# Kernel tuning notes

Hardware: AMD Instinct MI355X
Metric: run time of the kernel (lower is better)

## Reference

```python
import math
import jax, jax.numpy as jnp
import numpy as np

EPS = 1e-6
MAX_SCALE_LOG = math.log(100.0)

def rms_norm(x, scale, eps=EPS):
    # x * scale / rms(x), reduction over last dim
    ms = jnp.mean(jnp.square(x), axis=-1, keepdims=True)
    return x * (scale * jax.lax.rsqrt(ms + eps))

def axial_rope_theta(pos, n_heads, d_head, dtype):
    # freqs: linspace in log-space from pi to 10*pi, reshaped to [n_heads, d_head//4]
    f = np.exp(np.linspace(math.log(math.pi), math.log(10.0 * math.pi),
                           n_heads * d_head // 4 + 1)[:-1])
    freqs = jnp.asarray(f.reshape(d_head // 4, n_heads).T, dtype)  # [h, e/4]
    theta_h = pos[:, :, None, 0:1] * freqs  # [n, l, h, e/4]
    theta_w = pos[:, :, None, 1:2] * freqs  # [n, l, h, e/4]
    theta = jnp.concatenate([theta_h, theta_w], axis=-1)  # [n, l, h, e/2]
    return theta.transpose(0, 2, 1, 3)  # [n, h, l, e/2]

def apply_rotary(x, theta):
    d = theta.shape[-1]
    x1, x2, x3 = x[..., :d], x[..., d:2 * d], x[..., 2 * d:]
    cos, sin = jnp.cos(theta), jnp.sin(theta)
    return jnp.concatenate([x1 * cos - x2 * sin, x2 * cos + x1 * sin, x3], axis=-1)

def setup_inputs() -> dict:
    key = jax.random.key(0)
    ks = jax.random.split(key, 8)
    n, l, d_model, d_head = 2, 2048, 1024, 64
    n_heads = d_model // d_head
    x = jax.random.normal(ks[0], (n, l, d_model), jnp.float32)
    pos = jax.random.uniform(ks[1], (n, l, 2), jnp.float32)
    cond = jax.random.normal(ks[2], (n, 1, d_model), jnp.float32)
    # params (torch uses zero-init for w_cond/w_out; small random for a non-degenerate baseline)
    w_cond = jax.random.normal(ks[3], (d_model, d_model), jnp.float32) * 0.02
    w_qkv = jax.random.normal(ks[4], (d_model, 3 * d_model), jnp.float32) * (d_model ** -0.5)
    qk_scale = jnp.full((n_heads,), math.log(10.0), jnp.float32)
    w_out = jax.random.normal(ks[5], (d_model, d_model), jnp.float32) * 0.02
    return {"x": x, "pos": pos, "cond": cond, "w_cond": w_cond,
            "w_qkv": w_qkv, "qk_scale": qk_scale, "w_out": w_out}

def reference(x, pos, cond, w_cond, w_qkv, qk_scale, w_out):
    n, l, d_model = x.shape
    h = qk_scale.shape[0]
    e = d_model // h
    # AdaRMSNorm: scale = linear(cond) + 1
    xn = rms_norm(x, cond @ w_cond + 1.0)
    # QKV projection
    q, k, v = jnp.split(xn @ w_qkv, 3, axis=-1)
    to_heads = lambda t: t.reshape(n, l, h, e).transpose(0, 2, 1, 3)  # [n,h,l,e]
    q, k, v = to_heads(q), to_heads(k), to_heads(v)
    # QKNorm: per-head learned scale, rms over head dim
    s = jnp.exp(0.5 * jnp.minimum(qk_scale, MAX_SCALE_LOG) - 0.25 * math.log(e))
    q = rms_norm(q, s[:, None, None])
    k = rms_norm(k, s[:, None, None])
    # Axial RoPE
    theta = axial_rope_theta(pos, h, e, x.dtype)
    q = apply_rotary(q, theta)
    k = apply_rotary(k, theta)
    # SDPA (no mask)
    attn = jax.nn.softmax(jnp.einsum('nhqe,nhke->nhqk', q, k) / math.sqrt(e), axis=-1)
    o = jnp.einsum('nhqk,nhke->nhqe', attn, v)
    o = o.transpose(0, 2, 1, 3).reshape(n, l, d_model)
    return o @ w_out
```

## Files before the change

kernel.cpp:

```cpp
#include <hip/hip_runtime.h>

typedef unsigned short u16;
typedef unsigned int u32;
typedef short s16x8 __attribute__((ext_vector_type(8)));
typedef short s16x4 __attribute__((ext_vector_type(4)));
typedef float f32x4 __attribute__((ext_vector_type(4)));
typedef u32 u32x2 __attribute__((ext_vector_type(2)));

#define AS1 __attribute__((address_space(1)))
#define AS3 __attribute__((address_space(3)))

__device__ __forceinline__ float bf2f(u16 u) {
    union { unsigned int i; float f; } x; x.i = ((unsigned int)u) << 16; return x.f;
}
__device__ __forceinline__ u16 f2bf(float f) {
    union { float f; unsigned int i; } x; x.f = f;
    unsigned int r = (x.i + 0x7FFFu + ((x.i >> 16) & 1u)) >> 16;
    return (u16)r;
}
__device__ __forceinline__ void storeOut(u16* p, float v) { *p = f2bf(v); }
__device__ __forceinline__ void storeOut(float* p, float v) { *p = v; }
__device__ __forceinline__ float loadIn(const void* p, size_t i, int isf32) {
    return isf32 ? ((const float*)p)[i] : bf2f(((const u16*)p)[i]);
}
__device__ __forceinline__ float fexp2(float x) {
#if __has_builtin(__builtin_amdgcn_exp2f)
    return __builtin_amdgcn_exp2f(x);
#else
    return exp2f(x);
#endif
}
__device__ __forceinline__ u32 pack_bf(float a, float b) {
    u32 ua = __float_as_uint(a) + 0x8000u;
    u32 ub = __float_as_uint(b) + 0x8000u;
    return __builtin_amdgcn_perm(ub, ua, 0x07060302u);
}

__global__ __launch_bounds__(256) void detect_dtype(const u16* __restrict__ x,
                                                    int* __restrict__ flag) {
    __shared__ int cnt[4];
    const int tid = threadIdx.x;
    int c = 0;
    #pragma unroll
    for (int i = 0; i < 4; ++i) {
        const u16 u = x[tid * 4 + i];
        const int e = (u >> 7) & 0xFF;
        c += (e >= 101 && e <= 135) ? 1 : 0;
    }
    #pragma unroll
    for (int m = 1; m < 64; m <<= 1) c += __shfl_xor(c, m, 64);
    if ((tid & 63) == 0) cnt[tid >> 6] = c;
    __syncthreads();
    if (tid == 0) {
        const int t = cnt[0] + cnt[1] + cnt[2] + cnt[3];
        *flag = (t < 800) ? 1 : 0;
    }
}

__global__ __launch_bounds__(256) void cond_gemv(const void* __restrict__ cond,
                                                 const void* __restrict__ w,
                                                 float* __restrict__ out,
                                                 const int* __restrict__ flag) {
    const int isf32 = *flag;
    const int d  = blockIdx.x * 256 + threadIdx.x;
    const int n  = blockIdx.y;
    const int k0 = blockIdx.z * 64;
    float acc = 0.f;
    #pragma unroll 8
    for (int k = 0; k < 64; ++k)
        acc += loadIn(cond, n * 1024 + k0 + k, isf32) *
               loadIn(w, (size_t)(k0 + k) * 1024 + d, isf32);
    atomicAdd(out + n * 1024 + d, acc);
}

__global__ __launch_bounds__(256) void rmsnorm_x(const void* __restrict__ x,
                                                 const float* __restrict__ scl,
                                                 u16* __restrict__ xn,
                                                 const int* __restrict__ flag) {
    const int isf32 = *flag;
    const int tok = blockIdx.x;
    const int n = tok >> 11;
    u16* orow = xn + (size_t)tok * 1024;
    const int base = threadIdx.x * 4;
    float f0, f1, f2, f3;
    if (isf32) {
        const float4 v = *(const float4*)((const float*)x + (size_t)tok * 1024 + base);
        f0 = v.x; f1 = v.y; f2 = v.z; f3 = v.w;
    } else {
        s16x4 uv = *(const s16x4*)((const u16*)x + (size_t)tok * 1024 + base);
        f0 = bf2f((u16)uv[0]); f1 = bf2f((u16)uv[1]); f2 = bf2f((u16)uv[2]); f3 = bf2f((u16)uv[3]);
    }
    float ss = f0 * f0 + f1 * f1 + f2 * f2 + f3 * f3;
    #pragma unroll
    for (int m = 1; m < 64; m <<= 1) ss += __shfl_xor(ss, m, 64);
    __shared__ float red[4];
    const int wave = threadIdx.x >> 6, lane = threadIdx.x & 63;
    if (lane == 0) red[wave] = ss;
    __syncthreads();
    float ms = (red[0] + red[1] + red[2] + red[3]) * (1.f / 1024.f);
    float rinv = rsqrtf(ms + 1e-6f);
    orow[base + 0] = f2bf(f0 * (scl[n * 1024 + base + 0] + 1.f) * rinv);
    orow[base + 1] = f2bf(f1 * (scl[n * 1024 + base + 1] + 1.f) * rinv);
    orow[base + 2] = f2bf(f2 * (scl[n * 1024 + base + 2] + 1.f) * rinv);
    orow[base + 3] = f2bf(f3 * (scl[n * 1024 + base + 3] + 1.f) * rinv);
}

__global__ __launch_bounds__(256) void transpose_bf(const void* __restrict__ src,
                                                    u16* __restrict__ dst, int R, int C,
                                                    const int* __restrict__ flag) {
    const int isf32 = *flag;
    __shared__ u16 t[32][33];
    const int c0 = blockIdx.x * 32, r0 = blockIdx.y * 32;
    const int tx = threadIdx.x & 31, ty = threadIdx.x >> 5;
    #pragma unroll
    for (int i = 0; i < 4; ++i)
        t[ty + i * 8][tx] = f2bf(loadIn(src, (size_t)(r0 + ty + i * 8) * C + c0 + tx, isf32));
    __syncthreads();
    #pragma unroll
    for (int i = 0; i < 4; ++i)
        dst[(size_t)(c0 + ty + i * 8) * R + r0 + tx] = t[tx][ty + i * 8];
}

template <typename OutT>
__global__ __launch_bounds__(256) void gemm_bt(const u16* __restrict__ A,
                                               const u16* __restrict__ BT,
                                               OutT* __restrict__ C, int Nn, int K) {
    __shared__ u16 As[128 * 32];
    __shared__ u16 Bs[128 * 32];
    const int tid = threadIdx.x;
    const int wave = tid >> 6, lane = tid & 63;
    const int l15 = lane & 15, quad = lane >> 4;
    const int bm0 = blockIdx.y * 128, bn0 = blockIdx.x * 128;
    const int wr = wave >> 1, wc = wave & 1;
    f32x4 acc[4][4] = {};
    const int srow = lane >> 2;
    const int g = (lane & 3) ^ (srow & 3);
    for (int bk = 0; bk < K; bk += 32) {
        __syncthreads();
        #pragma unroll
        for (int p = 0; p < 2; ++p) {
            const int rowl = p * 64 + wave * 16 + srow;
            const u16* ga = A + (size_t)(bm0 + rowl) * K + bk + g * 8;
            u16* la = As + (p * 64 + wave * 16) * 32;
            __builtin_amdgcn_global_load_lds((const AS1 void*)ga, (AS3 void*)la, 16, 0, 0);
            const u16* gb = BT + (size_t)(bn0 + rowl) * K + bk + g * 8;
            u16* lb = Bs + (p * 64 + wave * 16) * 32;
            __builtin_amdgcn_global_load_lds((const AS1 void*)gb, (AS3 void*)lb, 16, 0, 0);
        }
        __syncthreads();
        s16x8 af[4], bfr[4];
        #pragma unroll
        for (int mt = 0; mt < 4; ++mt) {
            const int r = wr * 64 + mt * 16 + l15;
            af[mt] = *(const s16x8*)(As + r * 32 + ((quad ^ (r & 3)) << 3));
        }
        #pragma unroll
        for (int nt = 0; nt < 4; ++nt) {
            const int r = wc * 64 + nt * 16 + l15;
            bfr[nt] = *(const s16x8*)(Bs + r * 32 + ((quad ^ (r & 3)) << 3));
        }
        #pragma unroll
        for (int mt = 0; mt < 4; ++mt)
            #pragma unroll
            for (int nt = 0; nt < 4; ++nt)
                acc[mt][nt] = __builtin_amdgcn_mfma_f32_16x16x32_bf16(af[mt], bfr[nt], acc[mt][nt], 0, 0, 0);
    }
    #pragma unroll
    for (int mt = 0; mt < 4; ++mt)
        #pragma unroll
        for (int nt = 0; nt < 4; ++nt)
            #pragma unroll
            for (int r = 0; r < 4; ++r) {
                const int row = bm0 + wr * 64 + mt * 16 + quad * 4 + r;
                const int col = bn0 + wc * 64 + nt * 16 + l15;
                storeOut(C + (size_t)row * Nn + col, acc[mt][nt][r]);
            }
}

__global__ __launch_bounds__(256) void qkv_head(const u16* __restrict__ qkv,
                                                const void* __restrict__ pos,
                                                const void* __restrict__ qk_scale,
                                                u16* __restrict__ q_ws,
                                                u16* __restrict__ k_ws,
                                                u16* __restrict__ vtg,
                                                const int* __restrict__ flag) {
    const int isf32 = *flag;
    const int nh = blockIdx.y;
    const int n = nh >> 4, h = nh & 15;
    const int l0 = blockIdx.x * 64;
    const int tid = threadIdx.x;
    const int wave = tid >> 6, lane = tid & 63;

    const float qs = loadIn(qk_scale, h, isf32);
    const float s = __expf(0.5f * fminf(qs, 4.605170186f) - 1.039720771f);
    const float qmul = s * s * 0.125f * 1.44269504089f;
    const int j = lane & 31;
    const float t = (float)((j & 15) * 16 + h);
    const float freq = 3.14159265358979f * __expf(t * (2.302585093f / 256.f));
    const int pj = j >> 4;

    #pragma unroll 2
    for (int it = 0; it < 16; ++it) {
        const int l = l0 + wave * 16 + it;
        const int tok = n * 2048 + l;
        const u16* row = qkv + (size_t)tok * 3072;
        float qv = bf2f(row[h * 64 + lane]);
        float kv = bf2f(row[1024 + h * 64 + lane]);
        float q2 = qv * qv, k2 = kv * kv;
        #pragma unroll
        for (int m = 1; m < 64; m <<= 1) { q2 += __shfl_xor(q2, m, 64); k2 += __shfl_xor(k2, m, 64); }
        float qn = qv * rsqrtf(q2 * (1.f / 64.f) + 1e-6f) * qmul;
        float kn = kv * rsqrtf(k2 * (1.f / 64.f) + 1e-6f);
        const float p = loadIn(pos, tok * 2 + pj, isf32);
        const float th = p * freq;
        const float c = __cosf(th), sn = __sinf(th);
        const float pq = __shfl_xor(qn, 32, 64);
        const float pk = __shfl_xor(kn, 32, 64);
        float qr, kr;
        if (lane < 32) { qr = qn * c - pq * sn; kr = kn * c - pk * sn; }
        else           { qr = qn * c + pq * sn; kr = kn * c + pk * sn; }
        const size_t oidx = ((size_t)nh * 2048 + l) * 64 + lane;
        q_ws[oidx] = f2bf(qr);
        k_ws[oidx] = f2bf(kr);
    }

    __shared__ u16 tbuf[64][65];
    const u16* vsrc = qkv + (size_t)(n * 2048 + l0) * 3072 + 2048 + h * 64;
    #pragma unroll
    for (int it = 0; it < 16; ++it) {
        const int idx = it * 256 + tid;
        const int r = idx >> 6, c = idx & 63;
        tbuf[r][c] = vsrc[(size_t)r * 3072 + c];
    }
    __syncthreads();
    u16* dst = vtg + (size_t)nh * 131072 + l0;
    #pragma unroll
    for (int it = 0; it < 16; ++it) {
        const int idx = it * 256 + tid;
        const int er = idx >> 6, lc = idx & 63;
        dst[(size_t)er * 2048 + lc] = tbuf[lc][er];
    }
}

__global__ __launch_bounds__(256, 2) void attn5(const u16* __restrict__ Q,
                                                const u16* __restrict__ K,
                                                const u16* __restrict__ Vtg,
                                                u16* __restrict__ O) {
    __shared__ u16 Ks[2][64 * 64];
    __shared__ u16 Vt[3][64 * 64];
    __shared__ u16 Ps[4][32 * 72];
    const int nh = blockIdx.y;
    const int q0 = blockIdx.x * 128;
    const int tid = threadIdx.x;
    const int wave = tid >> 6, lane = tid & 63;
    const int l15 = lane & 15, quad = lane >> 4;
    const size_t hb = (size_t)nh * 2048 * 64;
    const u16* Vbase = Vtg + (size_t)nh * 131072;
    const int dr0 = tid >> 3;
    const int dd  = tid & 7;

    s16x8 qf[2][2];
    #pragma unroll
    for (int qg = 0; qg < 2; ++qg)
        #pragma unroll
        for (int kc = 0; kc < 2; ++kc)
            qf[qg][kc] = *(const s16x8*)(Q + hb + (size_t)(q0 + wave * 32 + qg * 16 + l15) * 64 + kc * 32 + quad * 8);

    f32x4 Oacc[2][4] = {};
    float lacc[2] = {0.f, 0.f};
    u16* Pw = Ps[wave];

    #pragma unroll
    for (int it = 0; it < 2; ++it) {
        const int row = it * 32 + dr0;
        const int g = dd ^ (row & 7);
        __builtin_amdgcn_global_load_lds(
            (const AS1 void*)(K + hb + (size_t)row * 64 + g * 8),
            (AS3 void*)(Ks[0] + (it * 256 + wave * 64) * 8), 16, 0, 0);
        __builtin_amdgcn_global_load_lds(
            (const AS1 void*)(Vbase + (size_t)row * 2048 + g * 8),
            (AS3 void*)(Vt[0] + (it * 256 + wave * 64) * 8), 16, 0, 0);
    }
    __syncthreads();

    int vprev = 2, vcur = 0, vnxt = 1;
    s16x8 pf[2][2];

    for (int i = 0; i < 32; ++i) {
        const int kcur = i & 1;
        if (i < 31) {
            const int kbn = (i + 1) * 64;
            #pragma unroll
            for (int it = 0; it < 2; ++it) {
                const int row = it * 32 + dr0;
                const int g = dd ^ (row & 7);
                __builtin_amdgcn_global_load_lds(
                    (const AS1 void*)(K + hb + (size_t)(kbn + row) * 64 + g * 8),
                    (AS3 void*)(Ks[kcur ^ 1] + (it * 256 + wave * 64) * 8), 16, 0, 0);
                __builtin_amdgcn_global_load_lds(
                    (const AS1 void*)(Vbase + (size_t)row * 2048 + kbn + g * 8),
                    (AS3 void*)(Vt[vnxt] + (it * 256 + wave * 64) * 8), 16, 0, 0);
            }
        }
        if (i > 0) {
            #pragma unroll
            for (int kc = 0; kc < 2; ++kc) {
                pf[kc][0] = *(const s16x8*)(Pw + l15 * 72 + kc * 32 + quad * 8);
                pf[kc][1] = *(const s16x8*)(Pw + (16 + l15) * 72 + kc * 32 + quad * 8);
            }
        }
        f32x4 S[2][4];
        #pragma unroll
        for (int qg = 0; qg < 2; ++qg)
            #pragma unroll
            for (int kt = 0; kt < 4; ++kt) {
                S[qg][kt][0] = -15.f; S[qg][kt][1] = -15.f;
                S[qg][kt][2] = -15.f; S[qg][kt][3] = -15.f;
            }
        #pragma unroll
        for (int kt = 0; kt < 4; ++kt) {
            const int r = kt * 16 + l15;
            #pragma unroll
            for (int kc = 0; kc < 2; ++kc) {
                const s16x8 kf = *(const s16x8*)(Ks[kcur] + r * 64 + (((kc * 4 + quad) ^ (r & 7)) << 3));
                S[0][kt] = __builtin_amdgcn_mfma_f32_16x16x32_bf16(kf, qf[0][kc], S[0][kt], 0, 0, 0);
                S[1][kt] = __builtin_amdgcn_mfma_f32_16x16x32_bf16(kf, qf[1][kc], S[1][kt], 0, 0, 0);
            }
        }
        if (i > 0) {
            #pragma unroll
            for (int kc = 0; kc < 2; ++kc)
                #pragma unroll
                for (int nto = 0; nto < 4; ++nto) {
                    const int e = nto * 16 + l15;
                    const s16x8 vf = *(const s16x8*)(Vt[vprev] + e * 64 + (((kc * 4 + quad) ^ (e & 7)) << 3));
                    Oacc[0][nto] = __builtin_amdgcn_mfma_f32_16x16x32_bf16(pf[kc][0], vf, Oacc[0][nto], 0, 0, 0);
                    Oacc[1][nto] = __builtin_amdgcn_mfma_f32_16x16x32_bf16(pf[kc][1], vf, Oacc[1][nto], 0, 0, 0);
                }
        }
        #pragma unroll
        for (int qg = 0; qg < 2; ++qg) {
            float rs = 0.f;
            #pragma unroll
            for (int kt = 0; kt < 4; ++kt) {
                const float e0 = fexp2(S[qg][kt][0]);
                const float e1 = fexp2(S[qg][kt][1]);
                const float e2 = fexp2(S[qg][kt][2]);
                const float e3 = fexp2(S[qg][kt][3]);
                rs += (e0 + e1) + (e2 + e3);
                u32x2 pk2;
                pk2[0] = pack_bf(e0, e1);
                pk2[1] = pack_bf(e2, e3);
                *(u32x2*)(Pw + (qg * 16 + l15) * 72 + kt * 16 + quad * 4) = pk2;
            }
            lacc[qg] += rs;
        }
        const int tmp = vprev; vprev = vcur; vcur = vnxt; vnxt = tmp;
        if (i < 31) __syncthreads();
    }

    #pragma unroll
    for (int kc = 0; kc < 2; ++kc) {
        pf[kc][0] = *(const s16x8*)(Pw + l15 * 72 + kc * 32 + quad * 8);
        pf[kc][1] = *(const s16x8*)(Pw + (16 + l15) * 72 + kc * 32 + quad * 8);
    }
    #pragma unroll
    for (int kc = 0; kc < 2; ++kc)
        #pragma unroll
        for (int nto = 0; nto < 4; ++nto) {
            const int e = nto * 16 + l15;
            const s16x8 vf = *(const s16x8*)(Vt[vprev] + e * 64 + (((kc * 4 + quad) ^ (e & 7)) << 3));
            Oacc[0][nto] = __builtin_amdgcn_mfma_f32_16x16x32_bf16(pf[kc][0], vf, Oacc[0][nto], 0, 0, 0);
            Oacc[1][nto] = __builtin_amdgcn_mfma_f32_16x16x32_bf16(pf[kc][1], vf, Oacc[1][nto], 0, 0, 0);
        }

    #pragma unroll
    for (int qg = 0; qg < 2; ++qg) {
        lacc[qg] += __shfl_xor(lacc[qg], 16, 64);
        lacc[qg] += __shfl_xor(lacc[qg], 32, 64);
    }

    const int n = nh >> 4, h = nh & 15;
    #pragma unroll
    for (int qg = 0; qg < 2; ++qg)
        #pragma unroll
        for (int r = 0; r < 4; ++r) {
            const float linv = 1.f / __shfl(lacc[qg], quad * 4 + r, 64);
            const int qrow = q0 + wave * 32 + qg * 16 + quad * 4 + r;
            #pragma unroll
            for (int nto = 0; nto < 4; ++nto)
                O[((size_t)n * 2048 + qrow) * 1024 + h * 64 + nto * 16 + l15] = f2bf(Oacc[qg][nto][r] * linv);
        }
}

extern "C" void kernel_launch(void* const* d_in, const int* in_sizes, int n_in,
                              void* d_out, int out_size, void* d_ws, size_t ws_size,
                              hipStream_t stream) {
    const void* x        = d_in[0];
    const void* pos      = d_in[1];
    const void* cond     = d_in[2];
    const void* w_cond   = d_in[3];
    const void* w_qkv    = d_in[4];
    const void* qk_scale = d_in[5];
    const void* w_out    = d_in[6];

    char* ws = (char*)d_ws;
    constexpr size_t OFS_SCALE = 0;
    constexpr size_t OFS_FLAG  = 8192;
    constexpr size_t OFS_XN    = 16384;
    constexpr size_t OFS_WQKVT = OFS_XN    + 8388608;
    constexpr size_t OFS_WOUTT = OFS_WQKVT + 6291456;
    constexpr size_t OFS_QKV   = OFS_WOUTT + 2097152;
    constexpr size_t OFS_Q     = OFS_QKV   + 25165824;
    constexpr size_t OFS_K     = OFS_Q     + 8388608;
    constexpr size_t OFS_VT    = OFS_K     + 8388608;
    constexpr size_t OFS_O     = OFS_VT    + 8388608;

    float* scale = (float*)(ws + OFS_SCALE);
    int*   flag  = (int*)(ws + OFS_FLAG);
    u16* xn    = (u16*)(ws + OFS_XN);
    u16* wqkvT = (u16*)(ws + OFS_WQKVT);
    u16* woutT = (u16*)(ws + OFS_WOUTT);
    u16* qkv   = (u16*)(ws + OFS_QKV);
    u16* qws   = (u16*)(ws + OFS_Q);
    u16* kws   = (u16*)(ws + OFS_K);
    u16* vtg   = (u16*)(ws + OFS_VT);
    u16* ows   = (u16*)(ws + OFS_O);

    detect_dtype<<<dim3(1), 256, 0, stream>>>((const u16*)x, flag);
    hipMemsetAsync(scale, 0, 2 * 1024 * sizeof(float), stream);
    cond_gemv<<<dim3(4, 2, 16), 256, 0, stream>>>(cond, w_cond, scale, flag);
    rmsnorm_x<<<dim3(4096), 256, 0, stream>>>(x, scale, xn, flag);
    transpose_bf<<<dim3(96, 32), 256, 0, stream>>>(w_qkv, wqkvT, 1024, 3072, flag);
    transpose_bf<<<dim3(32, 32), 256, 0, stream>>>(w_out, woutT, 1024, 1024, flag);
    gemm_bt<u16><<<dim3(24, 32), 256, 0, stream>>>(xn, wqkvT, qkv, 3072, 1024);
    qkv_head<<<dim3(32, 32), 256, 0, stream>>>(qkv, pos, qk_scale, qws, kws, vtg, flag);
    attn5<<<dim3(16, 32), 256, 0, stream>>>(qws, kws, vtg, ows);
    gemm_bt<float><<<dim3(8, 32), 256, 0, stream>>>(ows, woutT, (float*)d_out, 1024, 1024);
}
```

Baseline: 239.5 us.

## Split attention over two KV halves with combine pass, smaller output GEMM tiles

Attention now splits the key range in two across a grid z dimension, doubling the block count from 512 to 1024 to fill the CUs better, and writes unnormalized fp32 partial outputs and row sums. A new combine kernel adds the two halves and normalizes. The software-pipelined P·V overlap is replaced by a simpler in-iteration P·V with double-buffered V, and occupancy is raised to 3 blocks. The output projection uses a new 128x64-tile GEMM to launch more blocks. The cost is extra fp32 partial traffic and one more launch. The combine appears to rely on no running-max subtraction, so the partial sums can be added directly.

Measured after the change: 246.7 us. +3.0%, slower.

```diff
diff --git a/kernel.cpp b/kernel.cpp
--- a/kernel.cpp
+++ b/kernel.cpp
@@ -140,12 +140,12 @@
         #pragma unroll
         for (int p = 0; p < 2; ++p) {
             const int rowl = p * 64 + wave * 16 + srow;
-            const u16* ga = A + (size_t)(bm0 + rowl) * K + bk + g * 8;
-            u16* la = As + (p * 64 + wave * 16) * 32;
-            __builtin_amdgcn_global_load_lds((const AS1 void*)ga, (AS3 void*)la, 16, 0, 0);
-            const u16* gb = BT + (size_t)(bn0 + rowl) * K + bk + g * 8;
-            u16* lb = Bs + (p * 64 + wave * 16) * 32;
-            __builtin_amdgcn_global_load_lds((const AS1 void*)gb, (AS3 void*)lb, 16, 0, 0);
+            __builtin_amdgcn_global_load_lds(
+                (const AS1 void*)(A + (size_t)(bm0 + rowl) * K + bk + g * 8),
+                (AS3 void*)(As + (p * 64 + wave * 16) * 32), 16, 0, 0);
+            __builtin_amdgcn_global_load_lds(
+                (const AS1 void*)(BT + (size_t)(bn0 + rowl) * K + bk + g * 8),
+                (AS3 void*)(Bs + (p * 64 + wave * 16) * 32), 16, 0, 0);
         }
         __syncthreads();
         s16x8 af[4], bfr[4];
@@ -173,6 +173,64 @@
             for (int r = 0; r < 4; ++r) {
                 const int row = bm0 + wr * 64 + mt * 16 + quad * 4 + r;
                 const int col = bn0 + wc * 64 + nt * 16 + l15;
+                storeOut(C + (size_t)row * Nn + col, acc[mt][nt][r]);
+            }
+}
+
+template <typename OutT>
+__global__ __launch_bounds__(256) void gemm_bt64(const u16* __restrict__ A,
+                                                 const u16* __restrict__ BT,
+                                                 OutT* __restrict__ C, int Nn, int K) {
+    __shared__ u16 As[128 * 32];
+    __shared__ u16 Bs[64 * 32];
+    const int tid = threadIdx.x;
+    const int wave = tid >> 6, lane = tid & 63;
+    const int l15 = lane & 15, quad = lane >> 4;
+    const int bm0 = blockIdx.y * 128, bn0 = blockIdx.x * 64;
+    f32x4 acc[2][4] = {};
+    const int srow = lane >> 2;
+    const int g = (lane & 3) ^ (srow & 3);
+    for (int bk = 0; bk < K; bk += 32) {
+        __syncthreads();
+        #pragma unroll
+        for (int p = 0; p < 2; ++p) {
+            const int rowl = p * 64 + wave * 16 + srow;
+            __builtin_amdgcn_global_load_lds(
+                (const AS1 void*)(A + (size_t)(bm0 + rowl) * K + bk + g * 8),
+                (AS3 void*)(As + (p * 64 + wave * 16) * 32), 16, 0, 0);
+        }
+        {
+            const int rowb = wave * 16 + srow;
+            __builtin_amdgcn_global_load_lds(
+                (const AS1 void*)(BT + (size_t)(bn0 + rowb) * K + bk + g * 8),
+                (AS3 void*)(Bs + (wave * 16) * 32), 16, 0, 0);
+        }
+        __syncthreads();
+        s16x8 af[2], bfr[4];
+        #pragma unroll
+        for (int mt = 0; mt < 2; ++mt) {
+            const int r = wave * 32 + mt * 16 + l15;
+            af[mt] = *(const s16x8*)(As + r * 32 + ((quad ^ (r & 3)) << 3));
+        }
+        #pragma unroll
+        for (int nt = 0; nt < 4; ++nt) {
+            const int r = nt * 16 + l15;
+            bfr[nt] = *(const s16x8*)(Bs + r * 32 + ((quad ^ (r & 3)) << 3));
+        }
+        #pragma unroll
+        for (int mt = 0; mt < 2; ++mt)
+            #pragma unroll
+            for (int nt = 0; nt < 4; ++nt)
+                acc[mt][nt] = __builtin_amdgcn_mfma_f32_16x16x32_bf16(af[mt], bfr[nt], acc[mt][nt], 0, 0, 0);
+    }
+    #pragma unroll
+    for (int mt = 0; mt < 2; ++mt)
+        #pragma unroll
+        for (int nt = 0; nt < 4; ++nt)
+            #pragma unroll
+            for (int r = 0; r < 4; ++r) {
+                const int row = bm0 + wave * 32 + mt * 16 + quad * 4 + r;
+                const int col = bn0 + nt * 16 + l15;
                 storeOut(C + (size_t)row * Nn + col, acc[mt][nt][r]);
             }
 }
@@ -242,15 +300,18 @@
     }
 }
 
-__global__ __launch_bounds__(256, 2) void attn5(const u16* __restrict__ Q,
+__global__ __launch_bounds__(256, 3) void attn6(const u16* __restrict__ Q,
                                                 const u16* __restrict__ K,
                                                 const u16* __restrict__ Vtg,
-                                                u16* __restrict__ O) {
+                                                float* __restrict__ Opart,
+                                                float* __restrict__ lpart) {
     __shared__ u16 Ks[2][64 * 64];
-    __shared__ u16 Vt[3][64 * 64];
+    __shared__ u16 Vt[2][64 * 64];
     __shared__ u16 Ps[4][32 * 72];
     const int nh = blockIdx.y;
     const int q0 = blockIdx.x * 128;
+    const int ks = blockIdx.z;
+    const int kb0 = ks * 1024;
     const int tid = threadIdx.x;
     const int wave = tid >> 6, lane = tid & 63;
     const int l15 = lane & 15, quad = lane >> 4;
@@ -275,40 +336,33 @@
         const int row = it * 32 + dr0;
         const int g = dd ^ (row & 7);
         __builtin_amdgcn_global_load_lds(
-            (const AS1 void*)(K + hb + (size_t)row * 64 + g * 8),
+            (const AS1 void*)(K + hb + (size_t)(kb0 + row) * 64 + g * 8),
             (AS3 void*)(Ks[0] + (it * 256 + wave * 64) * 8), 16, 0, 0);
         __builtin_amdgcn_global_load_lds(
-            (const AS1 void*)(Vbase + (size_t)row * 2048 + g * 8),
+            (const AS1 void*)(Vbase + (size_t)row * 2048 + kb0 + g * 8),
             (AS3 void*)(Vt[0] + (it * 256 + wave * 64) * 8), 16, 0, 0);
     }
     __syncthreads();
 
-    int vprev = 2, vcur = 0, vnxt = 1;
-    s16x8 pf[2][2];
-
-    for (int i = 0; i < 32; ++i) {
-        const int kcur = i & 1;
-        if (i < 31) {
-            const int kbn = (i + 1) * 64;
+    for (int i = 0; i < 16; ++i) {
+        const int cur = i & 1;
+        const int kb = kb0 + i * 64;
+        if (i < 15) {
+            const int nxt = cur ^ 1;
+            const int kbn = kb + 64;
             #pragma unroll
             for (int it = 0; it < 2; ++it) {
                 const int row = it * 32 + dr0;
                 const int g = dd ^ (row & 7);
                 __builtin_amdgcn_global_load_lds(
                     (const AS1 void*)(K + hb + (size_t)(kbn + row) * 64 + g * 8),
-                    (AS3 void*)(Ks[kcur ^ 1] + (it * 256 + wave * 64) * 8), 16, 0, 0);
+                    (AS3 void*)(Ks[nxt] + (it * 256 + wave * 64) * 8), 16, 0, 0);
                 __builtin_amdgcn_global_load_lds(
                     (const AS1 void*)(Vbase + (size_t)row * 2048 + kbn + g * 8),
-                    (AS3 void*)(Vt[vnxt] + (it * 256 + wave * 64) * 8), 16, 0, 0);
-            }
-        }
-        if (i > 0) {
-            #pragma unroll
-            for (int kc = 0; kc < 2; ++kc) {
-                pf[kc][0] = *(const s16x8*)(Pw + l15 * 72 + kc * 32 + quad * 8);
-                pf[kc][1] = *(const s16x8*)(Pw + (16 + l15) * 72 + kc * 32 + quad * 8);
-            }
-        }
+                    (AS3 void*)(Vt[nxt] + (it * 256 + wave * 64) * 8), 16, 0, 0);
+            }
+        }
+
         f32x4 S[2][4];
         #pragma unroll
         for (int qg = 0; qg < 2; ++qg)
@@ -322,22 +376,12 @@
             const int r = kt * 16 + l15;
             #pragma unroll
             for (int kc = 0; kc < 2; ++kc) {
-                const s16x8 kf = *(const s16x8*)(Ks[kcur] + r * 64 + (((kc * 4 + quad) ^ (r & 7)) << 3));
+                const s16x8 kf = *(const s16x8*)(Ks[cur] + r * 64 + (((kc * 4 + quad) ^ (r & 7)) << 3));
                 S[0][kt] = __builtin_amdgcn_mfma_f32_16x16x32_bf16(kf, qf[0][kc], S[0][kt], 0, 0, 0);
                 S[1][kt] = __builtin_amdgcn_mfma_f32_16x16x32_bf16(kf, qf[1][kc], S[1][kt], 0, 0, 0);
             }
         }
-        if (i > 0) {
-            #pragma unroll
-            for (int kc = 0; kc < 2; ++kc)
-                #pragma unroll
-                for (int nto = 0; nto < 4; ++nto) {
-                    const int e = nto * 16 + l15;
-                    const s16x8 vf = *(const s16x8*)(Vt[vprev] + e * 64 + (((kc * 4 + quad) ^ (e & 7)) << 3));
-                    Oacc[0][nto] = __builtin_amdgcn_mfma_f32_16x16x32_bf16(pf[kc][0], vf, Oacc[0][nto], 0, 0, 0);
-                    Oacc[1][nto] = __builtin_amdgcn_mfma_f32_16x16x32_bf16(pf[kc][1], vf, Oacc[1][nto], 0, 0, 0);
-                }
-        }
+
         #pragma unroll
         for (int qg = 0; qg < 2; ++qg) {
             float rs = 0.f;
@@ -355,24 +399,22 @@
             }
             lacc[qg] += rs;
         }
-        const int tmp = vprev; vprev = vcur; vcur = vnxt; vnxt = tmp;
-        if (i < 31) __syncthreads();
-    }
-
-    #pragma unroll
-    for (int kc = 0; kc < 2; ++kc) {
-        pf[kc][0] = *(const s16x8*)(Pw + l15 * 72 + kc * 32 + quad * 8);
-        pf[kc][1] = *(const s16x8*)(Pw + (16 + l15) * 72 + kc * 32 + quad * 8);
-    }
-    #pragma unroll
-    for (int kc = 0; kc < 2; ++kc)
-        #pragma unroll
-        for (int nto = 0; nto < 4; ++nto) {
-            const int e = nto * 16 + l15;
-            const s16x8 vf = *(const s16x8*)(Vt[vprev] + e * 64 + (((kc * 4 + quad) ^ (e & 7)) << 3));
-            Oacc[0][nto] = __builtin_amdgcn_mfma_f32_16x16x32_bf16(pf[kc][0], vf, Oacc[0][nto], 0, 0, 0);
-            Oacc[1][nto] = __builtin_amdgcn_mfma_f32_16x16x32_bf16(pf[kc][1], vf, Oacc[1][nto], 0, 0, 0);
-        }
+
+        #pragma unroll
+        for (int kc = 0; kc < 2; ++kc) {
+            const s16x8 pf0 = *(const s16x8*)(Pw + l15 * 72 + kc * 32 + quad * 8);
+            const s16x8 pf1 = *(const s16x8*)(Pw + (16 + l15) * 72 + kc * 32 + quad * 8);
+            #pragma unroll
+            for (int nto = 0; nto < 4; ++nto) {
+                const int e = nto * 16 + l15;
+                const s16x8 vf = *(const s16x8*)(Vt[cur] + e * 64 + (((kc * 4 + quad) ^ (e & 7)) << 3));
+                Oacc[0][nto] = __builtin_amdgcn_mfma_f32_16x16x32_bf16(pf0, vf, Oacc[0][nto], 0, 0, 0);
+                Oacc[1][nto] = __builtin_amdgcn_mfma_f32_16x16x32_bf16(pf1, vf, Oacc[1][nto], 0, 0, 0);
+            }
+        }
+
+        if (i < 15) __syncthreads();
+    }
 
     #pragma unroll
     for (int qg = 0; qg < 2; ++qg) {
@@ -380,17 +422,43 @@
         lacc[qg] += __shfl_xor(lacc[qg], 32, 64);
     }
 
-    const int n = nh >> 4, h = nh & 15;
+    const size_t pb = ((size_t)(ks * 32 + nh)) * 2048;
+    if (quad == 0) {
+        #pragma unroll
+        for (int qg = 0; qg < 2; ++qg)
+            lpart[pb + q0 + wave * 32 + qg * 16 + l15] = lacc[qg];
+    }
     #pragma unroll
     for (int qg = 0; qg < 2; ++qg)
         #pragma unroll
         for (int r = 0; r < 4; ++r) {
-            const float linv = 1.f / __shfl(lacc[qg], quad * 4 + r, 64);
             const int qrow = q0 + wave * 32 + qg * 16 + quad * 4 + r;
+            float* orow = Opart + (pb + qrow) * 64;
             #pragma unroll
             for (int nto = 0; nto < 4; ++nto)
-                O[((size_t)n * 2048 + qrow) * 1024 + h * 64 + nto * 16 + l15] = f2bf(Oacc[qg][nto][r] * linv);
-        }
+                orow[nto * 16 + l15] = Oacc[qg][nto][r];
+        }
+}
+
+__global__ __launch_bounds__(256) void combine_o(const float* __restrict__ Opart,
+                                                 const float* __restrict__ lpart,
+                                                 u16* __restrict__ O) {
+    constexpr size_t HS = (size_t)32 * 2048 * 64;
+    constexpr size_t LS = (size_t)32 * 2048;
+    const int tok = blockIdx.x;
+    const int n = tok >> 11, l = tok & 2047;
+    const int idx = threadIdx.x * 4;
+    const int h = idx >> 6;
+    const int nh = n * 16 + h;
+    const size_t base = ((size_t)nh * 2048 + l) * 64 + (idx & 63);
+    const float4 a = *(const float4*)(Opart + base);
+    const float4 b = *(const float4*)(Opart + HS + base);
+    const float inv = 1.f / (lpart[(size_t)nh * 2048 + l] + lpart[LS + (size_t)nh * 2048 + l]);
+    u16* o = O + (size_t)tok * 1024 + idx;
+    o[0] = f2bf((a.x + b.x) * inv);
+    o[1] = f2bf((a.y + b.y) * inv);
+    o[2] = f2bf((a.z + b.z) * inv);
+    o[3] = f2bf((a.w + b.w) * inv);
 }
 
 extern "C" void kernel_launch(void* const* d_in, const int* in_sizes, int n_in,
@@ -405,16 +473,19 @@
     const void* w_out    = d_in[6];
 
     char* ws = (char*)d_ws;
+    constexpr size_t MB = 1048576;
     constexpr size_t OFS_SCALE = 0;
     constexpr size_t OFS_FLAG  = 8192;
-    constexpr size_t OFS_XN    = 16384;
-    constexpr size_t OFS_WQKVT = OFS_XN    + 8388608;
-    constexpr size_t OFS_WOUTT = OFS_WQKVT + 6291456;
-    constexpr size_t OFS_QKV   = OFS_WOUTT + 2097152;
-    constexpr size_t OFS_Q     = OFS_QKV   + 25165824;
-    constexpr size_t OFS_K     = OFS_Q     + 8388608;
-    constexpr size_t OFS_VT    = OFS_K     + 8388608;
-    constexpr size_t OFS_O     = OFS_VT    + 8388608;
+    constexpr size_t OFS_WOUTT = 16384;
+    constexpr size_t OFS_Q     = OFS_WOUTT + 2 * MB;
+    constexpr size_t OFS_K     = OFS_Q     + 8 * MB;
+    constexpr size_t OFS_VT    = OFS_K     + 8 * MB;
+    constexpr size_t OFS_O     = OFS_VT    + 8 * MB;
+    constexpr size_t OFS_XN    = OFS_O     + 8 * MB;
+    constexpr size_t OFS_WQKVT = OFS_XN    + 8 * MB;
+    constexpr size_t OFS_QKV   = OFS_WQKVT + 6 * MB;
+    constexpr size_t OFS_OPART = OFS_XN;
+    constexpr size_t OFS_LPART = OFS_OPART + 32 * MB;
 
     float* scale = (float*)(ws + OFS_SCALE);
     int*   flag  = (int*)(ws + OFS_FLAG);
@@ -426,6 +497,8 @@
     u16* kws   = (u16*)(ws + OFS_K);
     u16* vtg   = (u16*)(ws + OFS_VT);
     u16* ows   = (u16*)(ws + OFS_O);
+    float* opart = (float*)(ws + OFS_OPART);
+    float* lpart = (float*)(ws + OFS_LPART);
 
     detect_dtype<<<dim3(1), 256, 0, stream>>>((const u16*)x, flag);
     hipMemsetAsync(scale, 0, 2 * 1024 * sizeof(float), stream);
@@ -435,6 +508,7 @@
     transpose_bf<<<dim3(32, 32), 256, 0, stream>>>(w_out, woutT, 1024, 1024, flag);
     gemm_bt<u16><<<dim3(24, 32), 256, 0, stream>>>(xn, wqkvT, qkv, 3072, 1024);
     qkv_head<<<dim3(32, 32), 256, 0, stream>>>(qkv, pos, qk_scale, qws, kws, vtg, flag);
-    attn5<<<dim3(16, 32), 256, 0, stream>>>(qws, kws, vtg, ows);
-    gemm_bt<float><<<dim3(8, 32), 256, 0, stream>>>(ows, woutT, (float*)d_out, 1024, 1024);
-}
+    attn6<<<dim3(16, 32, 2), 256, 0, stream>>>(qws, kws, vtg, opart, lpart);
+    combine_o<<<dim3(4096), 256, 0, stream>>>(opart, lpart, ows);
+    gemm_bt64<float><<<dim3(16, 32), 256, 0, stream>>>(ows, woutT, (float*)d_out, 1024, 1024);
+}
```
